# Optimization experiments

Measured on AMD Instinct MI355X. Metric: run time of the kernel, lower is better.

## Reference

```python
import jax, jax.numpy as jnp
import numpy as np

NUM_EXPERTS = 8
HIDDEN = 2048
INTER = 6144
TOKENS_PER_EXPERT = 1024


def setup_inputs() -> dict:
    key = jax.random.key(0)
    k1, k2, k3 = jax.random.split(key, 3)
    routed_tokens = jax.random.normal(k1, (NUM_EXPERTS * TOKENS_PER_EXPERT, HIDDEN), dtype=jnp.float32)
    # fused gate+up projection weight per expert: [E, D, 2*I]
    w_gate_up = jax.random.normal(k2, (NUM_EXPERTS, HIDDEN, 2 * INTER), dtype=jnp.float32) * (1.0 / np.sqrt(HIDDEN))
    # down projection weight per expert: [E, I, D]
    w_down = jax.random.normal(k3, (NUM_EXPERTS, INTER, HIDDEN), dtype=jnp.float32) * (1.0 / np.sqrt(INTER))
    return {"routed_tokens": routed_tokens, "w_gate_up": w_gate_up, "w_down": w_down}


def reference(routed_tokens, w_gate_up, w_down):
    E, D = NUM_EXPERTS, HIDDEN
    x = routed_tokens.reshape(E, -1, D)               # [E, T, D]
    gate_up = jnp.einsum('etd,edf->etf', x, w_gate_up)  # [E, T, 2I]
    gate, up = jnp.split(gate_up, 2, axis=-1)          # chunk(2, dim=-1)
    hidden = jax.nn.silu(gate) * up                    # [E, T, I]
    out = jnp.einsum('eti,eid->etd', hidden, w_down)   # [E, T, D]
    return out.reshape(-1, D)
```

## Files before the change

kernel.cpp:

```cpp
#include <hip/hip_runtime.h>
#include <hip/hip_bf16.h>

#define NUM_EXPERTS 8
#define HIDDEN      2048
#define INTER       6144
#define TOKENS      1024

typedef __bf16 bf16x8 __attribute__((ext_vector_type(8)));
typedef __bf16 bf16x4 __attribute__((ext_vector_type(4)));
typedef float  floatx4 __attribute__((ext_vector_type(4)));

__device__ __forceinline__ void load_lds16(const void* gp, void* lp) {
    __builtin_amdgcn_global_load_lds(
        (__attribute__((address_space(1))) void*)(gp),
        (__attribute__((address_space(3))) void*)(lp),
        16, 0, 0);
}

__global__ void cvt_f32_bf16(const float* __restrict__ in, __bf16* __restrict__ out, size_t n) {
    size_t i = ((size_t)blockIdx.x * blockDim.x + threadIdx.x) * 4;
    if (i + 3 < n) {
        float4 v = *(const float4*)(in + i);
        bf16x4 o;
        o[0] = (__bf16)v.x; o[1] = (__bf16)v.y; o[2] = (__bf16)v.z; o[3] = (__bf16)v.w;
        *(bf16x4*)(out + i) = o;
    }
}

__global__ void transpose_cvt(const float* __restrict__ in, __bf16* __restrict__ out,
                              int R, int C) {
    __shared__ __bf16 tile[64][66];
    const int tx = threadIdx.x & 63;
    const int ty = threadIdx.x >> 6;
    const int c0 = blockIdx.x * 64;
    const int r0 = blockIdx.y * 64;
    const float* inb = in + (size_t)blockIdx.z * (size_t)R * (size_t)C;
    __bf16* outb = out + (size_t)blockIdx.z * (size_t)R * (size_t)C;
    #pragma unroll
    for (int r = ty; r < 64; r += 4)
        tile[r][tx] = (__bf16)inb[(size_t)(r0 + r) * C + (c0 + tx)];
    __syncthreads();
    #pragma unroll
    for (int cc = ty; cc < 64; cc += 4)
        outb[(size_t)(c0 + cc) * R + (r0 + tx)] = tile[tx][cc];
}

__global__ void silu_mul(const __bf16* __restrict__ gu, __bf16* __restrict__ h) {
    size_t lin = ((size_t)blockIdx.x * blockDim.x + threadIdx.x) * 4;
    size_t row = lin / INTER;
    int    i   = (int)(lin % INTER);
    bf16x4 g4 = *(const bf16x4*)(gu + row * (2 * INTER) + i);
    bf16x4 u4 = *(const bf16x4*)(gu + row * (2 * INTER) + INTER + i);
    bf16x4 o;
    #pragma unroll
    for (int j = 0; j < 4; ++j) {
        float g = (float)g4[j];
        float u = (float)u4[j];
        float s = g / (1.f + __expf(-g));
        o[j] = (__bf16)(s * u);
    }
    *(bf16x4*)(h + row * INTER + i) = o;
}

#define BM 128
#define BN 128
#define BK 32

template <bool OUT_BF16>
__global__ void gemm_bt(const __bf16* __restrict__ A, const __bf16* __restrict__ Bt,
                        void* __restrict__ C, int M, int N, int K,
                        size_t sA, size_t sB, size_t sC) {
    __shared__ alignas(16) __bf16 As[BM * BK];
    __shared__ alignas(16) __bf16 Bs[BN * BK];

    const int tid  = threadIdx.x;
    const int wid  = tid >> 6;
    const int lane = tid & 63;
    const int lr   = lane & 15;
    const int lh   = lane >> 4;
    const int m0   = blockIdx.y * BM;
    const int n0   = blockIdx.x * BN;

    const __bf16* Ae = A  + (size_t)blockIdx.z * sA;
    const __bf16* Be = Bt + (size_t)blockIdx.z * sB;

    const int wm = (wid >> 1) * 64;
    const int wn = (wid & 1) * 64;

    floatx4 acc[4][4];
    #pragma unroll
    for (int i = 0; i < 4; ++i)
        #pragma unroll
        for (int j = 0; j < 4; ++j)
            acc[i][j] = floatx4{0.f, 0.f, 0.f, 0.f};

    const int segBase = wid * 2048;

    for (int kt = 0; kt < K; kt += BK) {
        #pragma unroll
        for (int c = 0; c < 2; ++c) {
            int L    = segBase + c * 1024 + lane * 16;
            int row  = L >> 6;
            int colb = L & 63;
            const char* gp = (const char*)(Ae + (size_t)(m0 + row) * K + kt) + colb;
            load_lds16(gp, (char*)As + segBase + c * 1024);
        }
        #pragma unroll
        for (int c = 0; c < 2; ++c) {
            int L    = segBase + c * 1024 + lane * 16;
            int row  = L >> 6;
            int colb = L & 63;
            const char* gp = (const char*)(Be + (size_t)(n0 + row) * K + kt) + colb;
            load_lds16(gp, (char*)Bs + segBase + c * 1024);
        }
        __syncthreads();

        bf16x8 a[4], b[4];
        #pragma unroll
        for (int mt = 0; mt < 4; ++mt)
            a[mt] = *(const bf16x8*)&As[(wm + mt * 16 + lr) * BK + lh * 8];
        #pragma unroll
        for (int nt = 0; nt < 4; ++nt)
            b[nt] = *(const bf16x8*)&Bs[(wn + nt * 16 + lr) * BK + lh * 8];

        #pragma unroll
        for (int mt = 0; mt < 4; ++mt)
            #pragma unroll
            for (int nt = 0; nt < 4; ++nt)
                acc[mt][nt] = __builtin_amdgcn_mfma_f32_16x16x32_bf16(
                    a[mt], b[nt], acc[mt][nt], 0, 0, 0);
        __syncthreads();
    }

    if constexpr (OUT_BF16) {
        __bf16* Ce = (__bf16*)C + (size_t)blockIdx.z * sC;
        #pragma unroll
        for (int mt = 0; mt < 4; ++mt)
            #pragma unroll
            for (int nt = 0; nt < 4; ++nt)
                #pragma unroll
                for (int v = 0; v < 4; ++v) {
                    int r = m0 + wm + mt * 16 + lh * 4 + v;
                    int c = n0 + wn + nt * 16 + lr;
                    Ce[(size_t)r * N + c] = (__bf16)acc[mt][nt][v];
                }
    } else {
        float* Ce = (float*)C + (size_t)blockIdx.z * sC;
        #pragma unroll
        for (int mt = 0; mt < 4; ++mt)
            #pragma unroll
            for (int nt = 0; nt < 4; ++nt)
                #pragma unroll
                for (int v = 0; v < 4; ++v) {
                    int r = m0 + wm + mt * 16 + lh * 4 + v;
                    int c = n0 + wn + nt * 16 + lr;
                    Ce[(size_t)r * N + c] = acc[mt][nt][v];
                }
    }
}

extern "C" void kernel_launch(void* const* d_in, const int* in_sizes, int n_in,
                              void* d_out, int out_size, void* d_ws, size_t ws_size,
                              hipStream_t stream) {
    const float* x   = (const float*)d_in[0];
    const float* wgu = (const float*)d_in[1];
    const float* wd  = (const float*)d_in[2];
    float* out = (float*)d_out;

    constexpr size_t E = NUM_EXPERTS, T = TOKENS, D = HIDDEN, I = INTER;

    char* ws = (char*)d_ws;
    __bf16* GU   = (__bf16*)ws;
    __bf16* WdT  = (__bf16*)ws;
    char*   regA = ws + 201326592;
    __bf16* Xb   = (__bf16*)regA;
    __bf16* WguT = (__bf16*)(regA + 33554432);
    __bf16* H    = (__bf16*)regA;

    cvt_f32_bf16<<<dim3(16384), dim3(256), 0, stream>>>(x, Xb, E * T * D);

    transpose_cvt<<<dim3(2 * I / 64, D / 64, E), dim3(256), 0, stream>>>(wgu, WguT, (int)D, (int)(2 * I));

    gemm_bt<true><<<dim3(2 * I / BN, T / BM, E), dim3(256), 0, stream>>>(
        Xb, WguT, GU, (int)T, (int)(2 * I), (int)D, T * D, 2 * I * D, T * 2 * I);

    silu_mul<<<dim3((unsigned)(E * T * I / 4 / 256)), dim3(256), 0, stream>>>(GU, H);

    transpose_cvt<<<dim3(D / 64, I / 64, E), dim3(256), 0, stream>>>(wd, WdT, (int)I, (int)D);

    gemm_bt<false><<<dim3(D / BN, T / BM, E), dim3(256), 0, stream>>>(
        H, WdT, out, (int)T, (int)D, (int)I, T * I, D * I, T * D);
}
```

Before: 2.233 ms.

## Fuse SiLU-mul into gate/up GEMM epilogue and vectorize swizzled transpose

The gate/up GEMM now loads matching gate and up weight rows into one B tile and applies SiLU(g)*u in its epilogue. This removes the 2I-wide bf16 intermediate write, the separate silu_mul kernel, and its reread. The weight transpose-convert kernel now uses float4 loads, an XOR-swizzled LDS tile and 16-byte bf16 stores in place of scalar accesses. The workspace layout is reorganized to match.

```diff
diff --git a/kernel.cpp b/kernel.cpp
--- a/kernel.cpp
+++ b/kernel.cpp
@@ -29,46 +29,137 @@
 
 __global__ void transpose_cvt(const float* __restrict__ in, __bf16* __restrict__ out,
                               int R, int C) {
-    __shared__ __bf16 tile[64][66];
-    const int tx = threadIdx.x & 63;
-    const int ty = threadIdx.x >> 6;
+    __shared__ __bf16 tile[64 * 64];
+    const int tid = threadIdx.x;
     const int c0 = blockIdx.x * 64;
     const int r0 = blockIdx.y * 64;
     const float* inb = in + (size_t)blockIdx.z * (size_t)R * (size_t)C;
     __bf16* outb = out + (size_t)blockIdx.z * (size_t)R * (size_t)C;
-    #pragma unroll
-    for (int r = ty; r < 64; r += 4)
-        tile[r][tx] = (__bf16)inb[(size_t)(r0 + r) * C + (c0 + tx)];
+
+    const int ci = (tid & 15) * 4;
+    const int rr = tid >> 4;
+    #pragma unroll
+    for (int p = 0; p < 4; ++p) {
+        int r = rr + 16 * p;
+        float4 v = *(const float4*)&inb[(size_t)(r0 + r) * C + (c0 + ci)];
+        bf16x4 o;
+        o[0] = (__bf16)v.x; o[1] = (__bf16)v.y; o[2] = (__bf16)v.z; o[3] = (__bf16)v.w;
+        int csw = ci ^ (8 * ((r >> 3) & 7));
+        *(bf16x4*)&tile[r * 64 + csw] = o;
+    }
     __syncthreads();
-    #pragma unroll
-    for (int cc = ty; cc < 64; cc += 4)
-        outb[(size_t)(c0 + cc) * R + (r0 + tx)] = tile[tx][cc];
-}
-
-__global__ void silu_mul(const __bf16* __restrict__ gu, __bf16* __restrict__ h) {
-    size_t lin = ((size_t)blockIdx.x * blockDim.x + threadIdx.x) * 4;
-    size_t row = lin / INTER;
-    int    i   = (int)(lin % INTER);
-    bf16x4 g4 = *(const bf16x4*)(gu + row * (2 * INTER) + i);
-    bf16x4 u4 = *(const bf16x4*)(gu + row * (2 * INTER) + INTER + i);
-    bf16x4 o;
-    #pragma unroll
-    for (int j = 0; j < 4; ++j) {
-        float g = (float)g4[j];
-        float u = (float)u4[j];
-        float s = g / (1.f + __expf(-g));
-        o[j] = (__bf16)(s * u);
-    }
-    *(bf16x4*)(h + row * INTER + i) = o;
+
+    const int cl = tid >> 3;
+    const int rb = (tid & 7) * 8;
+    #pragma unroll
+    for (int q = 0; q < 2; ++q) {
+        int c = cl + 32 * q;
+        bf16x8 o;
+        #pragma unroll
+        for (int j = 0; j < 8; ++j) {
+            int r = rb + j;
+            o[j] = tile[r * 64 + (c ^ (8 * ((r >> 3) & 7)))];
+        }
+        *(bf16x8*)&outb[(size_t)(c0 + c) * R + (r0 + rb)] = o;
+    }
 }
 
 #define BM 128
+#define BK 32
+
+__global__ void gemm1_silu(const __bf16* __restrict__ A, const __bf16* __restrict__ Bt,
+                           __bf16* __restrict__ H) {
+    __shared__ alignas(16) __bf16 As[BM * BK];
+    __shared__ alignas(16) __bf16 Bs[128 * BK];
+
+    const int tid  = threadIdx.x;
+    const int wid  = tid >> 6;
+    const int lane = tid & 63;
+    const int lr   = lane & 15;
+    const int lh   = lane >> 4;
+    const int m0   = blockIdx.y * BM;
+    const int n0   = blockIdx.x * 64;
+    const size_t z = blockIdx.z;
+
+    const __bf16* Ae = A  + z * (size_t)(TOKENS * HIDDEN);
+    const __bf16* Be = Bt + z * (size_t)(2 * INTER * HIDDEN);
+
+    const int wm = (wid >> 1) * 64;
+    const int wn = (wid & 1) * 32;
+
+    floatx4 accg[4][2], accu[4][2];
+    #pragma unroll
+    for (int i = 0; i < 4; ++i)
+        #pragma unroll
+        for (int j = 0; j < 2; ++j) {
+            accg[i][j] = floatx4{0.f, 0.f, 0.f, 0.f};
+            accu[i][j] = floatx4{0.f, 0.f, 0.f, 0.f};
+        }
+
+    const int segBase = wid * 2048;
+
+    for (int kt = 0; kt < HIDDEN; kt += BK) {
+        #pragma unroll
+        for (int c = 0; c < 2; ++c) {
+            int L    = segBase + c * 1024 + lane * 16;
+            int row  = L >> 6;
+            int colb = L & 63;
+            const char* gp = (const char*)(Ae + (size_t)(m0 + row) * HIDDEN + kt) + colb;
+            load_lds16(gp, (char*)As + segBase + c * 1024);
+        }
+        #pragma unroll
+        for (int c = 0; c < 2; ++c) {
+            int L    = segBase + c * 1024 + lane * 16;
+            int rr   = L >> 6;
+            int colb = L & 63;
+            int grow = (rr < 64) ? (n0 + rr) : (INTER + n0 + (rr - 64));
+            const char* gp = (const char*)(Be + (size_t)grow * HIDDEN + kt) + colb;
+            load_lds16(gp, (char*)Bs + segBase + c * 1024);
+        }
+        __syncthreads();
+
+        bf16x8 a[4], bg[2], bu[2];
+        #pragma unroll
+        for (int mt = 0; mt < 4; ++mt)
+            a[mt] = *(const bf16x8*)&As[(wm + mt * 16 + lr) * BK + lh * 8];
+        #pragma unroll
+        for (int nt = 0; nt < 2; ++nt) {
+            bg[nt] = *(const bf16x8*)&Bs[(wn + nt * 16 + lr) * BK + lh * 8];
+            bu[nt] = *(const bf16x8*)&Bs[(64 + wn + nt * 16 + lr) * BK + lh * 8];
+        }
+
+        #pragma unroll
+        for (int mt = 0; mt < 4; ++mt)
+            #pragma unroll
+            for (int nt = 0; nt < 2; ++nt) {
+                accg[mt][nt] = __builtin_amdgcn_mfma_f32_16x16x32_bf16(
+                    a[mt], bg[nt], accg[mt][nt], 0, 0, 0);
+                accu[mt][nt] = __builtin_amdgcn_mfma_f32_16x16x32_bf16(
+                    a[mt], bu[nt], accu[mt][nt], 0, 0, 0);
+            }
+        __syncthreads();
+    }
+
+    __bf16* He = H + z * (size_t)(TOKENS * INTER);
+    #pragma unroll
+    for (int mt = 0; mt < 4; ++mt)
+        #pragma unroll
+        for (int nt = 0; nt < 2; ++nt)
+            #pragma unroll
+            for (int v = 0; v < 4; ++v) {
+                int r = m0 + wm + mt * 16 + lh * 4 + v;
+                int c = n0 + wn + nt * 16 + lr;
+                float g = accg[mt][nt][v];
+                float u = accu[mt][nt][v];
+                float s = g / (1.f + __expf(-g));
+                He[(size_t)r * INTER + c] = (__bf16)(s * u);
+            }
+}
+
 #define BN 128
-#define BK 32
-
-template <bool OUT_BF16>
+
 __global__ void gemm_bt(const __bf16* __restrict__ A, const __bf16* __restrict__ Bt,
-                        void* __restrict__ C, int M, int N, int K,
+                        float* __restrict__ C, int M, int N, int K,
                         size_t sA, size_t sB, size_t sC) {
     __shared__ alignas(16) __bf16 As[BM * BK];
     __shared__ alignas(16) __bf16 Bs[BN * BK];
@@ -132,31 +223,17 @@
         __syncthreads();
     }
 
-    if constexpr (OUT_BF16) {
-        __bf16* Ce = (__bf16*)C + (size_t)blockIdx.z * sC;
-        #pragma unroll
-        for (int mt = 0; mt < 4; ++mt)
-            #pragma unroll
-            for (int nt = 0; nt < 4; ++nt)
-                #pragma unroll
-                for (int v = 0; v < 4; ++v) {
-                    int r = m0 + wm + mt * 16 + lh * 4 + v;
-                    int c = n0 + wn + nt * 16 + lr;
-                    Ce[(size_t)r * N + c] = (__bf16)acc[mt][nt][v];
-                }
-    } else {
-        float* Ce = (float*)C + (size_t)blockIdx.z * sC;
-        #pragma unroll
-        for (int mt = 0; mt < 4; ++mt)
-            #pragma unroll
-            for (int nt = 0; nt < 4; ++nt)
-                #pragma unroll
-                for (int v = 0; v < 4; ++v) {
-                    int r = m0 + wm + mt * 16 + lh * 4 + v;
-                    int c = n0 + wn + nt * 16 + lr;
-                    Ce[(size_t)r * N + c] = acc[mt][nt][v];
-                }
-    }
+    float* Ce = C + (size_t)blockIdx.z * sC;
+    #pragma unroll
+    for (int mt = 0; mt < 4; ++mt)
+        #pragma unroll
+        for (int nt = 0; nt < 4; ++nt)
+            #pragma unroll
+            for (int v = 0; v < 4; ++v) {
+                int r = m0 + wm + mt * 16 + lh * 4 + v;
+                int c = n0 + wn + nt * 16 + lr;
+                Ce[(size_t)r * N + c] = acc[mt][nt][v];
+            }
 }
 
 extern "C" void kernel_launch(void* const* d_in, const int* in_sizes, int n_in,
@@ -170,24 +247,21 @@
     constexpr size_t E = NUM_EXPERTS, T = TOKENS, D = HIDDEN, I = INTER;
 
     char* ws = (char*)d_ws;
-    __bf16* GU   = (__bf16*)ws;
-    __bf16* WdT  = (__bf16*)ws;
-    char*   regA = ws + 201326592;
-    __bf16* Xb   = (__bf16*)regA;
-    __bf16* WguT = (__bf16*)(regA + 33554432);
-    __bf16* H    = (__bf16*)regA;
+    __bf16* Xb   = (__bf16*)ws;
+    __bf16* H    = (__bf16*)(ws + 33554432);
+    __bf16* WguT = (__bf16*)(ws + 134217728);
+    __bf16* WdT  = (__bf16*)(ws + 134217728);
 
     cvt_f32_bf16<<<dim3(16384), dim3(256), 0, stream>>>(x, Xb, E * T * D);
 
-    transpose_cvt<<<dim3(2 * I / 64, D / 64, E), dim3(256), 0, stream>>>(wgu, WguT, (int)D, (int)(2 * I));
-
-    gemm_bt<true><<<dim3(2 * I / BN, T / BM, E), dim3(256), 0, stream>>>(
-        Xb, WguT, GU, (int)T, (int)(2 * I), (int)D, T * D, 2 * I * D, T * 2 * I);
-
-    silu_mul<<<dim3((unsigned)(E * T * I / 4 / 256)), dim3(256), 0, stream>>>(GU, H);
-
-    transpose_cvt<<<dim3(D / 64, I / 64, E), dim3(256), 0, stream>>>(wd, WdT, (int)I, (int)D);
-
-    gemm_bt<false><<<dim3(D / BN, T / BM, E), dim3(256), 0, stream>>>(
+    transpose_cvt<<<dim3(2 * I / 64, D / 64, E), dim3(256), 0, stream>>>(
+        wgu, WguT, (int)D, (int)(2 * I));
+
+    gemm1_silu<<<dim3(I / 64, T / BM, E), dim3(256), 0, stream>>>(Xb, WguT, H);
+
+    transpose_cvt<<<dim3(D / 64, I / 64, E), dim3(256), 0, stream>>>(
+        wd, WdT, (int)I, (int)D);
+
+    gemm_bt<<<dim3(D / BN, T / BM, E), dim3(256), 0, stream>>>(
         H, WdT, out, (int)T, (int)D, (int)I, T * I, D * I, T * D);
 }
```

New measurement: 2.142 ms. -4.0%, faster.
